# Optimization experiments

Hardware: AMD Instinct MI355X
Metric: run time of the kernel (lower is better)

The kernel has to match this reference:

```python
import jax, jax.numpy as jnp
import numpy as np

D_MODEL, NHEAD, INT_DIM = 1024, 16, 4096
HEAD_DIM = D_MODEL // NHEAD
EPS = 1e-5


def _layernorm(x, gamma, beta):
    mu = jnp.mean(x, axis=-1, keepdims=True)
    var = jnp.var(x, axis=-1, keepdims=True)
    return (x - mu) * jax.lax.rsqrt(var + EPS) * gamma + beta


def setup_inputs() -> dict:
    key = jax.random.key(0)
    ks = jax.random.split(key, 16)
    B, T = 2, 2048
    s = 0.02
    inp = {
        'x': jax.random.normal(ks[0], (B, T, D_MODEL), dtype=jnp.float32),
        'Wq': jax.random.normal(ks[1], (D_MODEL, D_MODEL), dtype=jnp.float32) * s,
        'bq': jnp.zeros((D_MODEL,), jnp.float32),
        'Wk': jax.random.normal(ks[2], (D_MODEL, D_MODEL), dtype=jnp.float32) * s,
        'bk': jnp.zeros((D_MODEL,), jnp.float32),
        'Wv': jax.random.normal(ks[3], (D_MODEL, D_MODEL), dtype=jnp.float32) * s,
        'bv': jnp.zeros((D_MODEL,), jnp.float32),
        'Wo': jax.random.normal(ks[4], (D_MODEL, D_MODEL), dtype=jnp.float32) * s,
        'bo': jnp.zeros((D_MODEL,), jnp.float32),
        'ln1_g': jnp.ones((D_MODEL,), jnp.float32),
        'ln1_b': jnp.zeros((D_MODEL,), jnp.float32),
        'ln2_g': jnp.ones((D_MODEL,), jnp.float32),
        'ln2_b': jnp.zeros((D_MODEL,), jnp.float32),
        'W1': jax.random.normal(ks[5], (D_MODEL, INT_DIM), dtype=jnp.float32) * s,
        'b1': jnp.zeros((INT_DIM,), jnp.float32),
        'W2': jax.random.normal(ks[6], (INT_DIM, D_MODEL), dtype=jnp.float32) * s,
        'b2': jnp.zeros((D_MODEL,), jnp.float32),
    }
    return inp


def reference(x, Wq, bq, Wk, bk, Wv, bv, Wo, bo, ln1_g, ln1_b, ln2_g, ln2_b, W1, b1, W2, b2):
    B, T, D = x.shape
    # projections
    q = (x @ Wq + bq).reshape(B, T, NHEAD, HEAD_DIM).transpose(0, 2, 1, 3)
    k = (x @ Wk + bk).reshape(B, T, NHEAD, HEAD_DIM).transpose(0, 2, 1, 3)
    v = (x @ Wv + bv).reshape(B, T, NHEAD, HEAD_DIM).transpose(0, 2, 1, 3)
    # attention: [B,H,T,T] scores, softmax over keys
    scores = jnp.einsum('bhqd,bhkd->bhqk', q, k) / jnp.sqrt(jnp.float32(HEAD_DIM))
    attn = jax.nn.softmax(scores, axis=-1)
    out = jnp.einsum('bhqk,bhkd->bhqd', attn, v)
    out = out.transpose(0, 2, 1, 3).reshape(B, T, D)
    attn_output = out @ Wo + bo
    # residual + layernorm 1
    h = _layernorm(x + attn_output, ln1_g, ln1_b)
    # FFN
    ff = jax.nn.relu(h @ W1 + b1) @ W2 + b2
    # residual + layernorm 2
    return _layernorm(h + ff, ln2_g, ln2_b)
```

## Files before the change

kernel.cpp:

```cpp
#include <hip/hip_runtime.h>
#include <cstdint>

#define DEVI __device__ __forceinline__

typedef float f32x4 __attribute__((ext_vector_type(4)));
typedef __bf16 bf16x8 __attribute__((ext_vector_type(8)));
typedef unsigned int u32x4v __attribute__((ext_vector_type(4)));
typedef unsigned short u16;
typedef unsigned int u32;
typedef unsigned long long u64;

#define LOG2E 1.44269504088896f
#define QSCALE (0.125f * LOG2E)

DEVI u16 bf16bits(float f) {
    u32 u = __builtin_bit_cast(u32, f);
    u32 r = u + 0x7fffu + ((u >> 16) & 1u);
    return (u16)(r >> 16);
}

DEVI u32 pack2bf(float a, float b) {
    u16 x = __builtin_bit_cast(u16, (__bf16)a);
    u16 y = __builtin_bit_cast(u16, (__bf16)b);
    return (u32)x | ((u32)y << 16);
}

DEVI float ex2(float x) {
    float r;
    asm("v_exp_f32 %0, %1" : "=v"(r) : "v"(x));
    return r;
}

DEVI void gload16(const void* g, const void* l) {
    __builtin_amdgcn_global_load_lds(
        (const __attribute__((address_space(1))) void*)(u64)(uintptr_t)g,
        (__attribute__((address_space(3))) void*)(u32)(uintptr_t)l,
        16, 0, 0);
}

#define VMCNT0_BARRIER()                                   \
    asm volatile("s_waitcnt vmcnt(0)" ::: "memory");       \
    __builtin_amdgcn_s_barrier()

__global__ __launch_bounds__(256)
void prep_kernel(const float* __restrict__ x, u16* __restrict__ xb,
                 const float* __restrict__ Wq, const float* __restrict__ Wk,
                 const float* __restrict__ Wv, const float* __restrict__ Wo,
                 u16* __restrict__ Wqt, u16* __restrict__ Wkt,
                 u16* __restrict__ Wvt, u16* __restrict__ Wot,
                 const float* __restrict__ W1, u16* __restrict__ W1t,
                 const float* __restrict__ W2, u16* __restrict__ W2t) {
    __shared__ float t[64][65];
    const int b = blockIdx.x;
    const int tid = threadIdx.x;
    if (b < 4096) {
        int i = b * 256 + tid;
        float4 v = ((const float4*)x)[i];
        ((uint2*)xb)[i] = make_uint2(pack2bf(v.x, v.y), pack2bf(v.z, v.w));
        return;
    }
    const float* src;
    u16* dst;
    int K_, N_, k0, n0;
    if (b < 5120) {
        int l = b - 4096;
        int z = l >> 8;
        l &= 255;
        src = z == 0 ? Wq : z == 1 ? Wk : z == 2 ? Wv : Wo;
        dst = z == 0 ? Wqt : z == 1 ? Wkt : z == 2 ? Wvt : Wot;
        K_ = 1024; N_ = 1024;
        k0 = (l & 15) * 64; n0 = (l >> 4) * 64;
    } else if (b < 6144) {
        int l = b - 5120;
        src = W1; dst = W1t; K_ = 1024; N_ = 4096;
        k0 = (l & 15) * 64; n0 = (l >> 4) * 64;
    } else {
        int l = b - 6144;
        src = W2; dst = W2t; K_ = 4096; N_ = 1024;
        k0 = (l & 63) * 64; n0 = (l >> 6) * 64;
    }
#pragma unroll
    for (int i = 0; i < 16; i++) {
        int idx = i * 256 + tid;
        int r = idx >> 6, c = idx & 63;
        t[r][c] = src[(u64)(k0 + r) * N_ + n0 + c];
    }
    __syncthreads();
#pragma unroll
    for (int i = 0; i < 16; i++) {
        int idx = i * 256 + tid;
        int r = idx >> 6, c = idx & 63;
        dst[(u64)(n0 + r) * K_ + k0 + c] = bf16bits(t[c][r]);
    }
}

enum { MODE_QK = 0, MODE_VT = 1, MODE_RESID = 2, MODE_RELU = 3 };

DEVI void gemm_core(const u16* __restrict__ A, const u16* __restrict__ Bt, int K_,
                    u16 (*ldsA)[128 * 64], u16 (*ldsB)[128 * 64],
                    f32x4 (&acc)[4][4], int m0, int n0) {
    const int tid = threadIdx.x;
    const int lane = tid & 63;
    const int wid = tid >> 6;
    const int wr = wid >> 1, wc = wid & 1;
    const int l15 = lane & 15, l4 = lane >> 4;
    const int srow = tid >> 3;
    const int sc = (tid & 7) ^ (srow & 7);

    const u16* ap[4];
    const u16* bp[4];
#pragma unroll
    for (int i = 0; i < 4; i++) {
        ap[i] = A + (u64)(m0 + i * 32 + srow) * K_ + sc * 8;
        bp[i] = Bt + (u64)(n0 + i * 32 + srow) * K_ + sc * 8;
    }

    auto stage = [&](int buf) {
#pragma unroll
        for (int i = 0; i < 4; i++) {
            gload16(ap[i], (const char*)ldsA[buf] + (i * 256 + tid) * 16);
            ap[i] += 64;
        }
#pragma unroll
        for (int i = 0; i < 4; i++) {
            gload16(bp[i], (const char*)ldsB[buf] + (i * 256 + tid) * 16);
            bp[i] += 64;
        }
    };

    auto compute = [&](const u16* A_, const u16* B_) {
#pragma unroll
        for (int ks = 0; ks < 2; ks++) {
            bf16x8 af[4], bfr[4];
#pragma unroll
            for (int mi = 0; mi < 4; mi++) {
                int row = wr * 64 + mi * 16 + l15;
                af[mi] = *(const bf16x8*)((const char*)A_ + row * 128 +
                                          (((ks * 4 + l4) ^ (row & 7)) * 16));
            }
#pragma unroll
            for (int ni = 0; ni < 4; ni++) {
                int row = wc * 64 + ni * 16 + l15;
                bfr[ni] = *(const bf16x8*)((const char*)B_ + row * 128 +
                                           (((ks * 4 + l4) ^ (row & 7)) * 16));
            }
            __builtin_amdgcn_s_setprio(1);
#pragma unroll
            for (int mi = 0; mi < 4; mi++)
#pragma unroll
                for (int ni = 0; ni < 4; ni++)
                    acc[mi][ni] = __builtin_amdgcn_mfma_f32_16x16x32_bf16(
                        af[mi], bfr[ni], acc[mi][ni], 0, 0, 0);
            __builtin_amdgcn_s_setprio(0);
        }
    };

    const int nk = K_ >> 6;
    stage(0);
    VMCNT0_BARRIER();
    for (int t = 0; t < nk; t += 2) {
        if (t + 1 < nk) stage(1);
        compute(ldsA[0], ldsB[0]);
        VMCNT0_BARRIER();
        if (t + 2 < nk) stage(0);
        compute(ldsA[1], ldsB[1]);
        VMCNT0_BARRIER();
    }
}

template <int MODE>
DEVI void gemm_epilogue(f32x4 (&acc)[4][4], const float* __restrict__ bias,
                        const float* __restrict__ resid, void* __restrict__ outp,
                        int N_, int m0, int n0, float scale) {
    const int tid = threadIdx.x;
    const int lane = tid & 63;
    const int wid = tid >> 6;
    const int wr = wid >> 1, wc = wid & 1;
    const int l15 = lane & 15, l4 = lane >> 4;
#pragma unroll
    for (int mi = 0; mi < 4; mi++) {
#pragma unroll
        for (int ni = 0; ni < 4; ni++) {
            const int n = n0 + wc * 64 + ni * 16 + l15;
            const float bv = bias[n];
            const int mb = m0 + wr * 64 + mi * 16 + l4 * 4;
            if (MODE == MODE_VT) {
                const int b = mb >> 11, t = mb & 2047;
                const int hh = n >> 6, d = n & 63;
                u32 lo = pack2bf(acc[mi][ni][0] + bv, acc[mi][ni][1] + bv);
                u32 hi = pack2bf(acc[mi][ni][2] + bv, acc[mi][ni][3] + bv);
                u64 idx = ((u64)((b << 4) + hh) * 64 + d) * 2048 + t;
                *(uint2*)((u16*)outp + idx) = make_uint2(lo, hi);
            } else {
#pragma unroll
                for (int r = 0; r < 4; r++) {
                    const int m = mb + r;
                    const float v = acc[mi][ni][r] + bv;
                    if (MODE == MODE_QK) {
                        const int b = m >> 11, t = m & 2047;
                        const int hh = n >> 6, d = n & 63;
                        ((u16*)outp)[(((u64)((b << 4) + hh) * 2048 + t) << 6) + d] =
                            bf16bits(v * scale);
                    } else if (MODE == MODE_RESID) {
                        const u64 i2 = (u64)m * N_ + n;
                        ((float*)outp)[i2] = v + resid[i2];
                    } else {
                        ((u16*)outp)[(u64)m * N_ + n] = bf16bits(fmaxf(v, 0.f));
                    }
                }
            }
        }
    }
}

template <int MODE>
__global__ __launch_bounds__(256, 2)
void gemm_kernel(const u16* __restrict__ A, const u16* __restrict__ Bt,
                 const float* __restrict__ bias, const float* __restrict__ resid,
                 void* __restrict__ outp, int N_, int K_) {
    __shared__ u16 ldsA[2][128 * 64];
    __shared__ u16 ldsB[2][128 * 64];
    const int m0 = blockIdx.x * 128;
    const int n0 = blockIdx.y * 128;
    f32x4 acc[4][4];
#pragma unroll
    for (int i = 0; i < 4; i++)
#pragma unroll
        for (int j = 0; j < 4; j++) acc[i][j] = (f32x4){0.f, 0.f, 0.f, 0.f};
    gemm_core(A, Bt, K_, ldsA, ldsB, acc, m0, n0);
    gemm_epilogue<MODE>(acc, bias, resid, outp, N_, m0, n0, 1.f);
}

__global__ __launch_bounds__(256, 2)
void gemm_qkv_kernel(const u16* __restrict__ A,
                     const u16* __restrict__ Wq, const u16* __restrict__ Wk,
                     const u16* __restrict__ Wv,
                     const float* __restrict__ bq, const float* __restrict__ bk,
                     const float* __restrict__ bv,
                     u16* __restrict__ Qo, u16* __restrict__ Ko, u16* __restrict__ Vo) {
    __shared__ u16 ldsA[2][128 * 64];
    __shared__ u16 ldsB[2][128 * 64];
    const int z = blockIdx.z;
    const u16* Bt = z == 0 ? Wq : z == 1 ? Wk : Wv;
    const float* bias = z == 0 ? bq : z == 1 ? bk : bv;
    const int m0 = blockIdx.x * 128;
    const int n0 = blockIdx.y * 128;
    f32x4 acc[4][4];
#pragma unroll
    for (int i = 0; i < 4; i++)
#pragma unroll
        for (int j = 0; j < 4; j++) acc[i][j] = (f32x4){0.f, 0.f, 0.f, 0.f};
    gemm_core(A, Bt, 1024, ldsA, ldsB, acc, m0, n0);
    if (z == 2)
        gemm_epilogue<MODE_VT>(acc, bias, nullptr, Vo, 1024, m0, n0, 1.f);
    else
        gemm_epilogue<MODE_QK>(acc, bias, nullptr, z == 0 ? Qo : Ko, 1024, m0, n0,
                               z == 0 ? QSCALE : 1.f);
}

__global__ __launch_bounds__(256, 2)
void gemm64_kernel(const u16* __restrict__ A, const u16* __restrict__ Bt,
                   const float* __restrict__ bias, const float* __restrict__ resid,
                   float* __restrict__ outp, int K_) {
    __shared__ u16 ldsA[3][128 * 64];
    __shared__ u16 ldsB[3][64 * 64];
    const int tid = threadIdx.x;
    const int lane = tid & 63;
    const int wid = tid >> 6;
    const int m0 = blockIdx.x * 128;
    const int n0 = blockIdx.y * 64;
    const int l15 = lane & 15, l4 = lane >> 4;
    const int srow = tid >> 3;
    const int sc = (tid & 7) ^ (srow & 7);

    const u16* ap[4];
    const u16* bp[2];
#pragma unroll
    for (int i = 0; i < 4; i++)
        ap[i] = A + (u64)(m0 + i * 32 + srow) * K_ + sc * 8;
#pragma unroll
    for (int i = 0; i < 2; i++)
        bp[i] = Bt + (u64)(n0 + i * 32 + srow) * K_ + sc * 8;

    auto stage = [&](int buf) {
#pragma unroll
        for (int i = 0; i < 4; i++) {
            gload16(ap[i], (const char*)ldsA[buf] + (i * 256 + tid) * 16);
            ap[i] += 64;
        }
#pragma unroll
        for (int i = 0; i < 2; i++) {
            gload16(bp[i], (const char*)ldsB[buf] + (i * 256 + tid) * 16);
            bp[i] += 64;
        }
    };

    f32x4 acc[2][4];
#pragma unroll
    for (int i = 0; i < 2; i++)
#pragma unroll
        for (int j = 0; j < 4; j++) acc[i][j] = (f32x4){0.f, 0.f, 0.f, 0.f};

    auto compute = [&](const u16* A_, const u16* B_) {
#pragma unroll
        for (int ks = 0; ks < 2; ks++) {
            bf16x8 af[2], bfr[4];
#pragma unroll
            for (int mi = 0; mi < 2; mi++) {
                int row = wid * 32 + mi * 16 + l15;
                af[mi] = *(const bf16x8*)((const char*)A_ + row * 128 +
                                          (((ks * 4 + l4) ^ (row & 7)) * 16));
            }
#pragma unroll
            for (int ni = 0; ni < 4; ni++) {
                int row = ni * 16 + l15;
                bfr[ni] = *(const bf16x8*)((const char*)B_ + row * 128 +
                                           (((ks * 4 + l4) ^ (row & 7)) * 16));
            }
            __builtin_amdgcn_s_setprio(1);
#pragma unroll
            for (int mi = 0; mi < 2; mi++)
#pragma unroll
                for (int ni = 0; ni < 4; ni++)
                    acc[mi][ni] = __builtin_amdgcn_mfma_f32_16x16x32_bf16(
                        af[mi], bfr[ni], acc[mi][ni], 0, 0, 0);
            __builtin_amdgcn_s_setprio(0);
        }
    };

    const int nk = K_ >> 6;
    stage(0);
    stage(1);
    int cb = 0, sb = 2;
    for (int t = 0; t < nk; t++) {
        if (t < nk - 1) {
            asm volatile("s_waitcnt vmcnt(6)" ::: "memory");
        } else {
            asm volatile("s_waitcnt vmcnt(0)" ::: "memory");
        }
        __builtin_amdgcn_s_barrier();
        if (t + 2 < nk) stage(sb);
        compute(ldsA[cb], ldsB[cb]);
        cb = (cb == 2) ? 0 : cb + 1;
        sb = (sb == 2) ? 0 : sb + 1;
    }

#pragma unroll
    for (int mi = 0; mi < 2; mi++) {
#pragma unroll
        for (int ni = 0; ni < 4; ni++) {
            const int n = n0 + ni * 16 + l15;
            const float bv = bias[n];
            const int mb = m0 + wid * 32 + mi * 16 + l4 * 4;
#pragma unroll
            for (int r = 0; r < 4; r++) {
                const u64 i2 = (u64)(mb + r) * 1024 + n;
                outp[i2] = acc[mi][ni][r] + bv + resid[i2];
            }
        }
    }
}

__global__ __launch_bounds__(256, 3)
void attn_kernel(const u16* __restrict__ Qg, const u16* __restrict__ Kg,
                 const u16* __restrict__ Vtg, u16* __restrict__ Og) {
    __shared__ u16 ldsK[3][64 * 64];
    __shared__ u16 ldsV[3][64 * 64];
    const int tid = threadIdx.x;
    const int lane = tid & 63;
    const int w = tid >> 6;
    const int l15 = lane & 15, l4 = lane >> 4;
    const int id = blockIdx.x;
    const int swz = (id & 7) * 128 + (id >> 3);
    const int bh = swz >> 5;
    const int qblk = swz & 31;
    const u64 kvbase = (u64)bh * 2048 * 64;
    const int qw0 = qblk * 64 + w * 16;

    const int srow = tid >> 3;
    const int sc8 = ((tid & 7) ^ (srow & 7)) * 8;
    const u16* kq0 = Kg + kvbase + (u64)srow * 64 + sc8;
    const u16* kq1 = Kg + kvbase + (u64)(srow + 32) * 64 + sc8;
    const u16* vq0 = Vtg + kvbase + (u64)srow * 2048 + sc8;
    const u16* vq1 = Vtg + kvbase + (u64)(srow + 32) * 2048 + sc8;

    auto stage = [&](int buf) {
        gload16(kq0, (const char*)ldsK[buf] + tid * 16);
        gload16(kq1, (const char*)ldsK[buf] + (256 + tid) * 16);
        gload16(vq0, (const char*)ldsV[buf] + tid * 16);
        gload16(vq1, (const char*)ldsV[buf] + (256 + tid) * 16);
        kq0 += 4096; kq1 += 4096; vq0 += 64; vq1 += 64;
    };

    bf16x8 aq[2];
#pragma unroll
    for (int ks = 0; ks < 2; ks++)
        aq[ks] = *(const bf16x8*)(Qg + kvbase + (u64)(qw0 + l15) * 64 + ks * 32 + l4 * 8);
    asm volatile("s_waitcnt vmcnt(0)" ::: "memory");

    stage(0);
    stage(1);

    const u32x4v onesw = {0x3F803F80u, 0x3F803F80u, 0x3F803F80u, 0x3F803F80u};
    const bf16x8 aones = __builtin_bit_cast(bf16x8, onesw);

    f32x4 acco[4];
#pragma unroll
    for (int i = 0; i < 4; i++) acco[i] = (f32x4){0.f, 0.f, 0.f, 0.f};
    f32x4 lacc = (f32x4){0.f, 0.f, 0.f, 0.f};

    auto tile_body = [&](const u16* K_, const u16* V_) {
        f32x4 sf[4];
#pragma unroll
        for (int f = 0; f < 4; f++) sf[f] = (f32x4){0.f, 0.f, 0.f, 0.f};
#pragma unroll
        for (int ks = 0; ks < 2; ks++) {
            bf16x8 ak[4];
#pragma unroll
            for (int f = 0; f < 4; f++) {
                int row = f * 16 + l15;
                ak[f] = *(const bf16x8*)((const char*)K_ + row * 128 +
                                         (((ks * 4 + l4) ^ (row & 7)) * 16));
            }
            __builtin_amdgcn_s_setprio(1);
#pragma unroll
            for (int f = 0; f < 4; f++)
                sf[f] = __builtin_amdgcn_mfma_f32_16x16x32_bf16(ak[f], aq[ks], sf[f], 0, 0, 0);
            __builtin_amdgcn_s_setprio(0);
        }

        u32 A[4], B[4];
#pragma unroll
        for (int f = 0; f < 4; f++) {
            float p0 = ex2(sf[f][0]);
            float p1 = ex2(sf[f][1]);
            float p2 = ex2(sf[f][2]);
            float p3 = ex2(sf[f][3]);
            A[f] = pack2bf(p0, p1);
            B[f] = pack2bf(p2, p3);
        }
        asm volatile("v_permlane32_swap_b32 %0, %1" : "+v"(A[0]), "+v"(A[1]));
        asm volatile("v_permlane16_swap_b32 %0, %1" : "+v"(A[0]), "+v"(A[1]));
        asm volatile("v_permlane32_swap_b32 %0, %1" : "+v"(B[0]), "+v"(B[1]));
        asm volatile("v_permlane16_swap_b32 %0, %1" : "+v"(B[0]), "+v"(B[1]));
        asm volatile("v_permlane32_swap_b32 %0, %1" : "+v"(A[2]), "+v"(A[3]));
        asm volatile("v_permlane16_swap_b32 %0, %1" : "+v"(A[2]), "+v"(A[3]));
        asm volatile("v_permlane32_swap_b32 %0, %1" : "+v"(B[2]), "+v"(B[3]));
        asm volatile("v_permlane16_swap_b32 %0, %1" : "+v"(B[2]), "+v"(B[3]));

#pragma unroll
        for (int ks = 0; ks < 2; ks++) {
            u32x4v pw = {A[2 * ks], B[2 * ks], A[2 * ks + 1], B[2 * ks + 1]};
            bf16x8 pfrag = __builtin_bit_cast(bf16x8, pw);
            bf16x8 av[4];
#pragma unroll
            for (int nf = 0; nf < 4; nf++) {
                int row = nf * 16 + l15;
                av[nf] = *(const bf16x8*)((const char*)V_ + row * 128 +
                                          (((ks * 4 + l4) ^ (row & 7)) * 16));
            }
            __builtin_amdgcn_s_setprio(1);
            lacc = __builtin_amdgcn_mfma_f32_16x16x32_bf16(aones, pfrag, lacc, 0, 0, 0);
#pragma unroll
            for (int nf = 0; nf < 4; nf++)
                acco[nf] = __builtin_amdgcn_mfma_f32_16x16x32_bf16(av[nf], pfrag, acco[nf], 0, 0, 0);
            __builtin_amdgcn_s_setprio(0);
        }
    };

    int cb = 0;
    int sb = 2;
    for (int t = 0; t < 31; t++) {
        asm volatile("s_waitcnt vmcnt(4)" ::: "memory");
        __builtin_amdgcn_s_barrier();
        if (t < 30) stage(sb);
        tile_body(ldsK[cb], ldsV[cb]);
        cb = (cb == 2) ? 0 : cb + 1;
        sb = (sb == 2) ? 0 : sb + 1;
    }
    asm volatile("s_waitcnt vmcnt(0)" ::: "memory");
    __builtin_amdgcn_s_barrier();
    tile_body(ldsK[cb], ldsV[cb]);

    const float inv = 1.f / lacc[0];

    const int b = bh >> 4, h = bh & 15;
    const int tq = qw0 + l15;
#pragma unroll
    for (int nf = 0; nf < 4; nf++) {
        const int d = nf * 16 + l4 * 4;
        u32 lo = pack2bf(acco[nf][0] * inv, acco[nf][1] * inv);
        u32 hi = pack2bf(acco[nf][2] * inv, acco[nf][3] * inv);
        *(uint2*)(Og + ((u64)(b * 2048 + tq) << 10) + h * 64 + d) = make_uint2(lo, hi);
    }
}

template <bool WB16>
__global__ __launch_bounds__(256, 4)
void ln_kernel(const float* __restrict__ in, const float* __restrict__ gam,
               const float* __restrict__ bet, float* __restrict__ outf,
               u16* __restrict__ outb) {
    __shared__ float red[2][4];
    const int row = blockIdx.x;
    const int tid = threadIdx.x;
    float4 v = ((const float4*)(in + (u64)row * 1024))[tid];
    float s = v.x + v.y + v.z + v.w;
    float sq = v.x * v.x + v.y * v.y + v.z * v.z + v.w * v.w;
#pragma unroll
    for (int sh = 1; sh < 64; sh <<= 1) {
        s += __shfl_xor(s, sh, 64);
        sq += __shfl_xor(sq, sh, 64);
    }
    if ((tid & 63) == 0) { red[0][tid >> 6] = s; red[1][tid >> 6] = sq; }
    __syncthreads();
    s = red[0][0] + red[0][1] + red[0][2] + red[0][3];
    sq = red[1][0] + red[1][1] + red[1][2] + red[1][3];
    float mu = s * (1.f / 1024.f);
    float var = sq * (1.f / 1024.f) - mu * mu;
    float inv = rsqrtf(var + 1e-5f);
    float4 g = ((const float4*)gam)[tid];
    float4 bb = ((const float4*)bet)[tid];
    float4 o;
    o.x = (v.x - mu) * inv * g.x + bb.x;
    o.y = (v.y - mu) * inv * g.y + bb.y;
    o.z = (v.z - mu) * inv * g.z + bb.z;
    o.w = (v.w - mu) * inv * g.w + bb.w;
    ((float4*)(outf + (u64)row * 1024))[tid] = o;
    if (WB16) {
        ((uint2*)(outb + (u64)row * 1024))[tid] = make_uint2(pack2bf(o.x, o.y), pack2bf(o.z, o.w));
    }
}

extern "C" void kernel_launch(void* const* d_in, const int* in_sizes, int n_in,
                              void* d_out, int out_size, void* d_ws, size_t ws_size,
                              hipStream_t stream) {
    (void)in_sizes; (void)n_in; (void)out_size; (void)ws_size;
    const float* x  = (const float*)d_in[0];
    const float* Wq = (const float*)d_in[1];
    const float* bq = (const float*)d_in[2];
    const float* Wk = (const float*)d_in[3];
    const float* bk = (const float*)d_in[4];
    const float* Wv = (const float*)d_in[5];
    const float* bv = (const float*)d_in[6];
    const float* Wo = (const float*)d_in[7];
    const float* bo = (const float*)d_in[8];
    const float* g1 = (const float*)d_in[9];
    const float* be1 = (const float*)d_in[10];
    const float* g2 = (const float*)d_in[11];
    const float* be2 = (const float*)d_in[12];
    const float* W1 = (const float*)d_in[13];
    const float* b1 = (const float*)d_in[14];
    const float* W2 = (const float*)d_in[15];
    const float* b2 = (const float*)d_in[16];

    char* ws = (char*)d_ws;
    const u64 MB = 1024ull * 1024ull;
    u16* xb    = (u16*)(ws + 0);
    u16* Wqt   = (u16*)(ws + 8 * MB);
    u16* Wkt   = (u16*)(ws + 10 * MB);
    u16* Wvt   = (u16*)(ws + 12 * MB);
    u16* Wot   = (u16*)(ws + 14 * MB);
    u16* W1t   = (u16*)(ws + 16 * MB);
    u16* W2t   = (u16*)(ws + 24 * MB);
    u16* Qb    = (u16*)(ws + 32 * MB);
    u16* Kb    = (u16*)(ws + 40 * MB);
    u16* Vtb   = (u16*)(ws + 48 * MB);
    u16* Ob    = (u16*)(ws + 56 * MB);
    float* pre1 = (float*)(ws + 64 * MB);
    float* hf  = (float*)(ws + 80 * MB);
    u16* hb    = (u16*)(ws + 96 * MB);
    u16* ffb   = (u16*)(ws + 104 * MB);
    float* pre2 = (float*)(ws + 64 * MB);

    prep_kernel<<<7168, 256, 0, stream>>>(x, xb, Wq, Wk, Wv, Wo,
                                          Wqt, Wkt, Wvt, Wot, W1, W1t, W2, W2t);

    gemm_qkv_kernel<<<dim3(32, 8, 3), 256, 0, stream>>>(xb, Wqt, Wkt, Wvt,
                                                        bq, bk, bv, Qb, Kb, Vtb);

    attn_kernel<<<1024, 256, 0, stream>>>(Qb, Kb, Vtb, Ob);

    gemm64_kernel<<<dim3(32, 16), 256, 0, stream>>>(Ob, Wot, bo, x, pre1, 1024);
    ln_kernel<true><<<4096, 256, 0, stream>>>(pre1, g1, be1, hf, hb);
    gemm_kernel<MODE_RELU><<<dim3(32, 32), 256, 0, stream>>>(hb, W1t, b1, nullptr, ffb, 4096, 1024);
    gemm64_kernel<<<dim3(32, 16), 256, 0, stream>>>(ffb, W2t, b2, hf, pre2, 4096);
    ln_kernel<false><<<4096, 256, 0, stream>>>(pre2, g2, be2, (float*)d_out, nullptr);
}
```

Before: 202.5 us.

## Triple-buffer A tiles in 128x128 GEMM core and read bf16 residual for FFN

The 128x128 GEMM core moves from a double-buffered loop that waits on vmcnt(0) at every step to a staggered pipeline. A tiles now use three LDS buffers and B tiles two, and a partial vmcnt(4) wait lets the next loads stay in flight while compute runs. Separately, the fp32 copy of the first layernorm output is no longer written, and the second-residual GEMM reads the bf16 copy instead, which cuts memory traffic. The bf16 residual lowers precision of the skip connection, and the larger LDS footprint may reduce occupancy for the two-blocks-per-CU launch bound.

```diff
diff --git a/kernel.cpp b/kernel.cpp
--- a/kernel.cpp
+++ b/kernel.cpp
@@ -19,6 +19,11 @@
     return (u16)(r >> 16);
 }
 
+DEVI float bf2f(u16 v) {
+    u32 u = (u32)v << 16;
+    return __builtin_bit_cast(float, u);
+}
+
 DEVI u32 pack2bf(float a, float b) {
     u16 x = __builtin_bit_cast(u16, (__bf16)a);
     u16 y = __builtin_bit_cast(u16, (__bf16)b);
@@ -37,10 +42,6 @@
         (__attribute__((address_space(3))) void*)(u32)(uintptr_t)l,
         16, 0, 0);
 }
-
-#define VMCNT0_BARRIER()                                   \
-    asm volatile("s_waitcnt vmcnt(0)" ::: "memory");       \
-    __builtin_amdgcn_s_barrier()
 
 __global__ __launch_bounds__(256)
 void prep_kernel(const float* __restrict__ x, u16* __restrict__ xb,
@@ -115,12 +116,14 @@
         bp[i] = Bt + (u64)(n0 + i * 32 + srow) * K_ + sc * 8;
     }
 
-    auto stage = [&](int buf) {
+    auto stageA = [&](int buf) {
 #pragma unroll
         for (int i = 0; i < 4; i++) {
             gload16(ap[i], (const char*)ldsA[buf] + (i * 256 + tid) * 16);
             ap[i] += 64;
         }
+    };
+    auto stageB = [&](int buf) {
 #pragma unroll
         for (int i = 0; i < 4; i++) {
             gload16(bp[i], (const char*)ldsB[buf] + (i * 256 + tid) * 16);
@@ -156,15 +159,22 @@
     };
 
     const int nk = K_ >> 6;
-    stage(0);
-    VMCNT0_BARRIER();
-    for (int t = 0; t < nk; t += 2) {
-        if (t + 1 < nk) stage(1);
-        compute(ldsA[0], ldsB[0]);
-        VMCNT0_BARRIER();
-        if (t + 2 < nk) stage(0);
-        compute(ldsA[1], ldsB[1]);
-        VMCNT0_BARRIER();
+    stageA(0);
+    stageB(0);
+    stageA(1);
+    int ca = 0, cbb = 0, sa = 2, sb = 1;
+    for (int t = 0; t < nk; t++) {
+        if (t < nk - 1) {
+            asm volatile("s_waitcnt vmcnt(4)" ::: "memory");
+        } else {
+            asm volatile("s_waitcnt vmcnt(0)" ::: "memory");
+        }
+        __builtin_amdgcn_s_barrier();
+        if (t + 1 < nk) { stageB(sb); sb ^= 1; }
+        if (t + 2 < nk) { stageA(sa); sa = (sa == 2) ? 0 : sa + 1; }
+        compute(ldsA[ca], ldsB[cbb]);
+        ca = (ca == 2) ? 0 : ca + 1;
+        cbb ^= 1;
     }
 }
 
@@ -218,7 +228,7 @@
 void gemm_kernel(const u16* __restrict__ A, const u16* __restrict__ Bt,
                  const float* __restrict__ bias, const float* __restrict__ resid,
                  void* __restrict__ outp, int N_, int K_) {
-    __shared__ u16 ldsA[2][128 * 64];
+    __shared__ u16 ldsA[3][128 * 64];
     __shared__ u16 ldsB[2][128 * 64];
     const int m0 = blockIdx.x * 128;
     const int n0 = blockIdx.y * 128;
@@ -238,7 +248,7 @@
                      const float* __restrict__ bq, const float* __restrict__ bk,
                      const float* __restrict__ bv,
                      u16* __restrict__ Qo, u16* __restrict__ Ko, u16* __restrict__ Vo) {
-    __shared__ u16 ldsA[2][128 * 64];
+    __shared__ u16 ldsA[3][128 * 64];
     __shared__ u16 ldsB[2][128 * 64];
     const int z = blockIdx.z;
     const u16* Bt = z == 0 ? Wq : z == 1 ? Wk : Wv;
@@ -258,9 +268,10 @@
                                z == 0 ? QSCALE : 1.f);
 }
 
+template <bool RB16>
 __global__ __launch_bounds__(256, 2)
 void gemm64_kernel(const u16* __restrict__ A, const u16* __restrict__ Bt,
-                   const float* __restrict__ bias, const float* __restrict__ resid,
+                   const float* __restrict__ bias, const void* __restrict__ resid,
                    float* __restrict__ outp, int K_) {
     __shared__ u16 ldsA[3][128 * 64];
     __shared__ u16 ldsB[3][64 * 64];
@@ -355,7 +366,9 @@
 #pragma unroll
             for (int r = 0; r < 4; r++) {
                 const u64 i2 = (u64)(mb + r) * 1024 + n;
-                outp[i2] = acc[mi][ni][r] + bv + resid[i2];
+                const float rv = RB16 ? bf2f(((const u16*)resid)[i2])
+                                      : ((const float*)resid)[i2];
+                outp[i2] = acc[mi][ni][r] + bv + rv;
             }
         }
     }
@@ -495,7 +508,7 @@
     }
 }
 
-template <bool WB16>
+template <bool WF32, bool WB16>
 __global__ __launch_bounds__(256, 4)
 void ln_kernel(const float* __restrict__ in, const float* __restrict__ gam,
                const float* __restrict__ bet, float* __restrict__ outf,
@@ -525,7 +538,7 @@
     o.y = (v.y - mu) * inv * g.y + bb.y;
     o.z = (v.z - mu) * inv * g.z + bb.z;
     o.w = (v.w - mu) * inv * g.w + bb.w;
-    ((float4*)(outf + (u64)row * 1024))[tid] = o;
+    if (WF32) ((float4*)(outf + (u64)row * 1024))[tid] = o;
     if (WB16) {
         ((uint2*)(outb + (u64)row * 1024))[tid] = make_uint2(pack2bf(o.x, o.y), pack2bf(o.z, o.w));
     }
@@ -567,10 +580,9 @@
     u16* Vtb   = (u16*)(ws + 48 * MB);
     u16* Ob    = (u16*)(ws + 56 * MB);
     float* pre1 = (float*)(ws + 64 * MB);
-    float* hf  = (float*)(ws + 80 * MB);
     u16* hb    = (u16*)(ws + 96 * MB);
     u16* ffb   = (u16*)(ws + 104 * MB);
-    float* pre2 = (float*)(ws + 64 * MB);
+    float* pre2 = (float*)(ws + 80 * MB);
 
     prep_kernel<<<7168, 256, 0, stream>>>(x, xb, Wq, Wk, Wv, Wo,
                                           Wqt, Wkt, Wvt, Wot, W1, W1t, W2, W2t);
@@ -580,9 +592,9 @@
 
     attn_kernel<<<1024, 256, 0, stream>>>(Qb, Kb, Vtb, Ob);
 
-    gemm64_kernel<<<dim3(32, 16), 256, 0, stream>>>(Ob, Wot, bo, x, pre1, 1024);
-    ln_kernel<true><<<4096, 256, 0, stream>>>(pre1, g1, be1, hf, hb);
+    gemm64_kernel<false><<<dim3(32, 16), 256, 0, stream>>>(Ob, Wot, bo, x, pre1, 1024);
+    ln_kernel<false, true><<<4096, 256, 0, stream>>>(pre1, g1, be1, nullptr, hb);
     gemm_kernel<MODE_RELU><<<dim3(32, 32), 256, 0, stream>>>(hb, W1t, b1, nullptr, ffb, 4096, 1024);
-    gemm64_kernel<<<dim3(32, 16), 256, 0, stream>>>(ffb, W2t, b2, hf, pre2, 4096);
-    ln_kernel<false><<<4096, 256, 0, stream>>>(pre2, g2, be2, (float*)d_out, nullptr);
-}
+    gemm64_kernel<true><<<dim3(32, 16), 256, 0, stream>>>(ffb, W2t, b2, hb, pre2, 4096);
+    ln_kernel<true, false><<<4096, 256, 0, stream>>>(pre2, g2, be2, (float*)d_out, nullptr);
+}
```

After: 202.2 us, median of 2. No clear change (-0.2%).
